# Performance work log

Hardware: AMD Instinct MI355X
Metric: run time of the kernel (lower is better)

Reference implementation:

```python
import jax, jax.numpy as jnp
import numpy as np

B, L, D, H = 4, 1024, 1024, 16
DH = D // H  # 64
TOPK = 32


def setup_inputs() -> dict:
    key = jax.random.key(0)
    ks = jax.random.split(key, 9)
    s = 1.0 / np.sqrt(D)
    return {
        "x": jax.random.normal(ks[0], (B, L, D), jnp.float32),
        "Wq": jax.random.normal(ks[1], (D, D), jnp.float32) * s,
        "bq": jax.random.normal(ks[2], (D,), jnp.float32) * 0.01,
        "Wk": jax.random.normal(ks[3], (D, D), jnp.float32) * s,
        "bk": jax.random.normal(ks[4], (D,), jnp.float32) * 0.01,
        "Wv": jax.random.normal(ks[5], (D, D), jnp.float32) * s,
        "bv": jax.random.normal(ks[6], (D,), jnp.float32) * 0.01,
        "Wo": jax.random.normal(ks[7], (D, D), jnp.float32) * s,
        "bo": jax.random.normal(ks[8], (D,), jnp.float32) * 0.01,
        "top_k": TOPK,
    }


def reference(x, Wq, bq, Wk, bk, Wv, bv, Wo, bo, top_k):
    b, l, _ = x.shape
    q = (x @ Wq + bq).reshape(b, l, H, DH)
    k = (x @ Wk + bk).reshape(b, l, H, DH)
    v = (x @ Wv + bv).reshape(b, l, H, DH)
    # scores: [B, i, j, h]
    scores = jnp.einsum('bihd,bjhd->bijh', q, k) / np.sqrt(DH).astype(np.float32)
    # softmax over axis 2 (j), as in the original (dim=2 of bijh)
    weights = jax.nn.softmax(scores, axis=2)
    if top_k is not None:
        # top-k along j: move j to last axis -> [B, i, h, j]
        w_t = jnp.swapaxes(weights, 2, 3)
        _, idx = jax.lax.top_k(w_t, top_k)
        mask = jnp.put_along_axis(jnp.zeros_like(w_t), idx, 1.0, axis=-1, inplace=False)
        w_t = w_t * mask
        w_t = w_t / (jnp.sum(w_t, axis=-1, keepdims=True) + 1e-8)
        weights = jnp.swapaxes(w_t, 2, 3)
    attn = jnp.einsum('bijh,bjhd->bihd', weights, v).reshape(b, l, D)
    return attn @ Wo + bo
```

## Files before the change

### kernel.cpp

```cpp
#include <hip/hip_runtime.h>
#include <math.h>

#define B_ 4
#define L_ 1024
#define D_ 1024
#define H_ 16
#define DH_ 64
#define M_ (B_*L_)

typedef _Float16 half8 __attribute__((ext_vector_type(8)));
typedef _Float16 half4 __attribute__((ext_vector_type(4)));
typedef float f32x4 __attribute__((ext_vector_type(4)));

#define MFMA16(a,b,c) __builtin_amdgcn_mfma_f32_16x16x32_f16(a, b, c, 0, 0, 0)

__global__ __launch_bounds__(256) void split_x(const float* __restrict__ x,
                                               _Float16* __restrict__ xh,
                                               _Float16* __restrict__ xl) {
  const int i = blockIdx.x * 256 + threadIdx.x;
  float4 v = ((const float4*)x)[i];
  const float a0 = v.x * 16.f, a1 = v.y * 16.f, a2 = v.z * 16.f, a3 = v.w * 16.f;
  const _Float16 h0 = (_Float16)a0, h1 = (_Float16)a1, h2 = (_Float16)a2, h3 = (_Float16)a3;
  half4 hv, lv;
  hv[0] = h0; hv[1] = h1; hv[2] = h2; hv[3] = h3;
  lv[0] = (_Float16)(a0 - (float)h0);
  lv[1] = (_Float16)(a1 - (float)h1);
  lv[2] = (_Float16)(a2 - (float)h2);
  lv[3] = (_Float16)(a3 - (float)h3);
  ((half4*)xh)[i] = hv;
  ((half4*)xl)[i] = lv;
}

__global__ __launch_bounds__(256) void split_wt(const float* __restrict__ W,
                                                _Float16* __restrict__ Wh,
                                                _Float16* __restrict__ Wl) {
  __shared__ float tile[64][65];
  const int t = threadIdx.x;
  const int tk = blockIdx.x & 15;
  const int tn = blockIdx.x >> 4;
  const int kr = t >> 2, ns = (t & 3) * 16;
  const float* src = W + (size_t)(tk * 64 + kr) * D_ + tn * 64 + ns;
  float4 v0 = ((const float4*)src)[0];
  float4 v1 = ((const float4*)src)[1];
  float4 v2 = ((const float4*)src)[2];
  float4 v3 = ((const float4*)src)[3];
  tile[ns + 0][kr] = v0.x;  tile[ns + 1][kr] = v0.y;  tile[ns + 2][kr] = v0.z;  tile[ns + 3][kr] = v0.w;
  tile[ns + 4][kr] = v1.x;  tile[ns + 5][kr] = v1.y;  tile[ns + 6][kr] = v1.z;  tile[ns + 7][kr] = v1.w;
  tile[ns + 8][kr] = v2.x;  tile[ns + 9][kr] = v2.y;  tile[ns + 10][kr] = v2.z; tile[ns + 11][kr] = v2.w;
  tile[ns + 12][kr] = v3.x; tile[ns + 13][kr] = v3.y; tile[ns + 14][kr] = v3.z; tile[ns + 15][kr] = v3.w;
  __syncthreads();
  const int nr = t >> 2, ks = (t & 3) * 16;
  const float* tr = &tile[nr][ks];
  half8 hv0, hv1, lv0, lv1;
#pragma unroll
  for (int i = 0; i < 8; i++) {
    const float s0 = tr[i] * 512.f;
    const float s1 = tr[i + 8] * 512.f;
    const _Float16 h0 = (_Float16)s0, h1 = (_Float16)s1;
    hv0[i] = h0; hv1[i] = h1;
    lv0[i] = (_Float16)(s0 - (float)h0);
    lv1[i] = (_Float16)(s1 - (float)h1);
  }
  _Float16* dh = Wh + (size_t)(tn * 64 + nr) * D_ + tk * 64 + ks;
  _Float16* dl = Wl + (size_t)(tn * 64 + nr) * D_ + tk * 64 + ks;
  *(half8*)dh = hv0; *(half8*)(dh + 8) = hv1;
  *(half8*)dl = lv0; *(half8*)(dl + 8) = lv1;
}

__device__ __forceinline__ void gemm_f16x3_body(
    const _Float16* __restrict__ Ah, const _Float16* __restrict__ Al,
    const _Float16* __restrict__ Bh, const _Float16* __restrict__ Bl,
    const float* __restrict__ bias, float* __restrict__ C) {
  __shared__ __align__(16) _Float16 sA[2][2][128][32];
  __shared__ __align__(16) _Float16 sB[2][2][128][32];
  const int t = threadIdx.x;
  const int lane = t & 63;
  const int wid = t >> 6;
  const int bm = blockIdx.y * 128;
  const int bn = blockIdx.x * 128;

  const int m0 = t >> 2, sp0 = t & 3;
  const int sl0 = sp0 ^ ((m0 >> 1) & 3);
  const int m1 = m0 + 64;
  const _Float16* gA0h = Ah + (size_t)(bm + m0) * D_ + sl0 * 8;
  const _Float16* gA1h = Ah + (size_t)(bm + m1) * D_ + sl0 * 8;
  const _Float16* gA0l = Al + (size_t)(bm + m0) * D_ + sl0 * 8;
  const _Float16* gA1l = Al + (size_t)(bm + m1) * D_ + sl0 * 8;
  const _Float16* gB0h = Bh + (size_t)(bn + m0) * D_ + sl0 * 8;
  const _Float16* gB1h = Bh + (size_t)(bn + m1) * D_ + sl0 * 8;
  const _Float16* gB0l = Bl + (size_t)(bn + m0) * D_ + sl0 * 8;
  const _Float16* gB1l = Bl + (size_t)(bn + m1) * D_ + sl0 * 8;

  half8 rA0h = *(const half8*)(gA0h);
  half8 rA1h = *(const half8*)(gA1h);
  half8 rA0l = *(const half8*)(gA0l);
  half8 rA1l = *(const half8*)(gA1l);
  half8 rB0h = *(const half8*)(gB0h);
  half8 rB1h = *(const half8*)(gB1h);
  half8 rB0l = *(const half8*)(gB0l);
  half8 rB1l = *(const half8*)(gB1l);
  *(half8*)&sA[0][0][m0][sp0 * 8] = rA0h;
  *(half8*)&sA[0][0][m1][sp0 * 8] = rA1h;
  *(half8*)&sA[0][1][m0][sp0 * 8] = rA0l;
  *(half8*)&sA[0][1][m1][sp0 * 8] = rA1l;
  *(half8*)&sB[0][0][m0][sp0 * 8] = rB0h;
  *(half8*)&sB[0][0][m1][sp0 * 8] = rB1h;
  *(half8*)&sB[0][1][m0][sp0 * 8] = rB0l;
  *(half8*)&sB[0][1][m1][sp0 * 8] = rB1l;
  __syncthreads();

  f32x4 acc[4][4];
#pragma unroll
  for (int i = 0; i < 4; i++)
#pragma unroll
    for (int j = 0; j < 4; j++) acc[i][j] = {0.f, 0.f, 0.f, 0.f};

  const int wr = wid >> 1, wc = wid & 1;
  const int l15 = lane & 15;
  const int soff = ((lane >> 4) ^ ((l15 >> 1) & 3)) * 8;

  int p = 0;
  for (int k0 = 0; k0 < 1024; k0 += 32) {
    const bool more = (k0 + 32) < 1024;
    if (more) {
      const int kk = k0 + 32;
      rA0h = *(const half8*)(gA0h + kk);
      rA1h = *(const half8*)(gA1h + kk);
      rA0l = *(const half8*)(gA0l + kk);
      rA1l = *(const half8*)(gA1l + kk);
      rB0h = *(const half8*)(gB0h + kk);
      rB1h = *(const half8*)(gB1h + kk);
      rB0l = *(const half8*)(gB0l + kk);
      rB1l = *(const half8*)(gB1l + kk);
    }
    half8 bh[4], bl[4];
#pragma unroll
    for (int ni = 0; ni < 4; ni++) {
      const int rb = wc * 64 + ni * 16 + l15;
      bh[ni] = *(const half8*)&sB[p][0][rb][soff];
      bl[ni] = *(const half8*)&sB[p][1][rb][soff];
    }
#pragma unroll
    for (int mi = 0; mi < 4; mi++) {
      const int ra = wr * 64 + mi * 16 + l15;
      const half8 ah = *(const half8*)&sA[p][0][ra][soff];
      const half8 al = *(const half8*)&sA[p][1][ra][soff];
#pragma unroll
      for (int ni = 0; ni < 4; ni++) {
        acc[mi][ni] = MFMA16(ah, bh[ni], acc[mi][ni]);
        acc[mi][ni] = MFMA16(ah, bl[ni], acc[mi][ni]);
        acc[mi][ni] = MFMA16(al, bh[ni], acc[mi][ni]);
      }
    }
    if (more) {
      const int q = p ^ 1;
      *(half8*)&sA[q][0][m0][sp0 * 8] = rA0h;
      *(half8*)&sA[q][0][m1][sp0 * 8] = rA1h;
      *(half8*)&sA[q][1][m0][sp0 * 8] = rA0l;
      *(half8*)&sA[q][1][m1][sp0 * 8] = rA1l;
      *(half8*)&sB[q][0][m0][sp0 * 8] = rB0h;
      *(half8*)&sB[q][0][m1][sp0 * 8] = rB1h;
      *(half8*)&sB[q][1][m0][sp0 * 8] = rB0l;
      *(half8*)&sB[q][1][m1][sp0 * 8] = rB1l;
      __syncthreads();
      p = q;
    }
  }

  const float inv = 1.0f / 8192.0f;
  const int orow = bm + wr * 64 + (lane >> 4) * 4;
  const int ocol = bn + wc * 64 + l15;
#pragma unroll
  for (int ni = 0; ni < 4; ni++) {
    const int col = ocol + ni * 16;
    const float bv = bias[col];
#pragma unroll
    for (int mi = 0; mi < 4; mi++) {
      const f32x4 a = acc[mi][ni];
#pragma unroll
      for (int r = 0; r < 4; r++)
        C[(size_t)(orow + mi * 16 + r) * D_ + col] = a[r] * inv + bv;
    }
  }
}

__global__ __launch_bounds__(256, 2) void gemm_qkv_f16(
    const _Float16* __restrict__ xh, const _Float16* __restrict__ xl,
    const _Float16* __restrict__ Whq, const _Float16* __restrict__ Wlq,
    const _Float16* __restrict__ Whk, const _Float16* __restrict__ Wlk,
    const _Float16* __restrict__ Whv, const _Float16* __restrict__ Wlv,
    const float* __restrict__ bq, const float* __restrict__ bk, const float* __restrict__ bv,
    float* __restrict__ qf, float* __restrict__ kf, float* __restrict__ vf) {
  const int z = blockIdx.z;
  const _Float16* Bh = (z == 0) ? Whq : (z == 1) ? Whk : Whv;
  const _Float16* Bl = (z == 0) ? Wlq : (z == 1) ? Wlk : Wlv;
  const float* bias = (z == 0) ? bq : (z == 1) ? bk : bv;
  float* C = (z == 0) ? qf : (z == 1) ? kf : vf;
  gemm_f16x3_body(xh, xl, Bh, Bl, bias, C);
}

__global__ __launch_bounds__(256, 2) void gemm_out_f16(
    const _Float16* __restrict__ ah, const _Float16* __restrict__ al,
    const _Float16* __restrict__ bh, const _Float16* __restrict__ bl,
    const float* __restrict__ bias, float* __restrict__ C) {
  gemm_f16x3_body(ah, al, bh, bl, bias, C);
}

__global__ __launch_bounds__(256) void transpose_k(const float* __restrict__ kf,
                                                   float* __restrict__ kT) {
  __shared__ float tile[64][65];
  const int t = threadIdx.x;
  const int c = blockIdx.x & 15;
  const int h = (blockIdx.x >> 4) & 15;
  const int b = blockIdx.x >> 8;
  const int j0 = c * 64;
  const int jr = t >> 2, ds = (t & 3) * 16;
  const float* src = kf + (size_t)(b * L_ + j0 + jr) * D_ + h * DH_ + ds;
  float4 v0 = ((const float4*)src)[0];
  float4 v1 = ((const float4*)src)[1];
  float4 v2 = ((const float4*)src)[2];
  float4 v3 = ((const float4*)src)[3];
  tile[ds + 0][jr] = v0.x;  tile[ds + 1][jr] = v0.y;  tile[ds + 2][jr] = v0.z;  tile[ds + 3][jr] = v0.w;
  tile[ds + 4][jr] = v1.x;  tile[ds + 5][jr] = v1.y;  tile[ds + 6][jr] = v1.z;  tile[ds + 7][jr] = v1.w;
  tile[ds + 8][jr] = v2.x;  tile[ds + 9][jr] = v2.y;  tile[ds + 10][jr] = v2.z; tile[ds + 11][jr] = v2.w;
  tile[ds + 12][jr] = v3.x; tile[ds + 13][jr] = v3.y; tile[ds + 14][jr] = v3.z; tile[ds + 15][jr] = v3.w;
  __syncthreads();
  const int dr = t >> 2, js = (t & 3) * 16;
  float* dst = kT + ((size_t)((b * 16 + h) * 16 + c)) * 4096 + dr * 64 + js;
  ((float4*)dst)[0] = *(const float4*)&tile[dr][js];
  ((float4*)dst)[1] = *(const float4*)&tile[dr][js + 4];
  ((float4*)dst)[2] = *(const float4*)&tile[dr][js + 8];
  ((float4*)dst)[3] = *(const float4*)&tile[dr][js + 12];
}

#define RFL(x) __int_as_float(__builtin_amdgcn_readfirstlane(__float_as_int(x)))
#define LQROW(r) \
  const float q##r##_0  = RFL(qsh[r][qo +  0]), q##r##_1  = RFL(qsh[r][qo +  1]), \
              q##r##_2  = RFL(qsh[r][qo +  2]), q##r##_3  = RFL(qsh[r][qo +  3]), \
              q##r##_4  = RFL(qsh[r][qo +  4]), q##r##_5  = RFL(qsh[r][qo +  5]), \
              q##r##_6  = RFL(qsh[r][qo +  6]), q##r##_7  = RFL(qsh[r][qo +  7]), \
              q##r##_8  = RFL(qsh[r][qo +  8]), q##r##_9  = RFL(qsh[r][qo +  9]), \
              q##r##_10 = RFL(qsh[r][qo + 10]), q##r##_11 = RFL(qsh[r][qo + 11]), \
              q##r##_12 = RFL(qsh[r][qo + 12]), q##r##_13 = RFL(qsh[r][qo + 13]), \
              q##r##_14 = RFL(qsh[r][qo + 14]), q##r##_15 = RFL(qsh[r][qo + 15]);
#define DOT16(r, sacc) \
  sacc = fmaf(kv0,  q##r##_0,  sacc); sacc = fmaf(kv1,  q##r##_1,  sacc); \
  sacc = fmaf(kv2,  q##r##_2,  sacc); sacc = fmaf(kv3,  q##r##_3,  sacc); \
  sacc = fmaf(kv4,  q##r##_4,  sacc); sacc = fmaf(kv5,  q##r##_5,  sacc); \
  sacc = fmaf(kv6,  q##r##_6,  sacc); sacc = fmaf(kv7,  q##r##_7,  sacc); \
  sacc = fmaf(kv8,  q##r##_8,  sacc); sacc = fmaf(kv9,  q##r##_9,  sacc); \
  sacc = fmaf(kv10, q##r##_10, sacc); sacc = fmaf(kv11, q##r##_11, sacc); \
  sacc = fmaf(kv12, q##r##_12, sacc); sacc = fmaf(kv13, q##r##_13, sacc); \
  sacc = fmaf(kv14, q##r##_14, sacc); sacc = fmaf(kv15, q##r##_15, sacc);

__global__ __launch_bounds__(256, 4) void attn_topk_f32(const float* __restrict__ qf,
                                                        const float* __restrict__ kT,
                                                        const float* __restrict__ vf,
                                                        _Float16* __restrict__ awh,
                                                        _Float16* __restrict__ awl) {
  __shared__ float part2[4][4][64][4];
  __shared__ float qsh[4][64];
  const int t = threadIdx.x;
  const int lane = t & 63;
  const int w = t >> 6;
  const int blk = blockIdx.x;
  const int ib = (blk & 255) * 4;
  const int h = (blk >> 8) & 15;
  const int b = blk >> 12;
  const size_t rowbase = (size_t)b * L_;

  { int r = t >> 6, d = t & 63; qsh[r][d] = qf[(rowbase + ib + r) * D_ + h * DH_ + d]; }
  __syncthreads();

  const int qo = 16 * w;
  LQROW(0) LQROW(1) LQROW(2) LQROW(3)

  const float* ktb = kT + ((size_t)(b * 16 + h) * 16) * 4096 + qo * 64;

  float sc[16];
#pragma unroll
  for (int s = 0; s < 4; ++s) {
#pragma unroll
    for (int c4 = 0; c4 < 4; ++c4) {
      const int c = s * 4 + c4;
      const float* kp = ktb + (size_t)c * 4096 + lane;
      const float kv0 = kp[0 * 64],  kv1 = kp[1 * 64],  kv2 = kp[2 * 64],  kv3 = kp[3 * 64],
                  kv4 = kp[4 * 64],  kv5 = kp[5 * 64],  kv6 = kp[6 * 64],  kv7 = kp[7 * 64],
                  kv8 = kp[8 * 64],  kv9 = kp[9 * 64],  kv10 = kp[10 * 64], kv11 = kp[11 * 64],
                  kv12 = kp[12 * 64], kv13 = kp[13 * 64], kv14 = kp[14 * 64], kv15 = kp[15 * 64];
      float p0 = 0.f, p1 = 0.f, p2 = 0.f, p3 = 0.f;
      DOT16(0, p0) DOT16(1, p1) DOT16(2, p2) DOT16(3, p3)
      part2[c4][0][lane][w] = p0;
      part2[c4][1][lane][w] = p1;
      part2[c4][2][lane][w] = p2;
      part2[c4][3][lane][w] = p3;
    }
    __syncthreads();
#pragma unroll
    for (int c4 = 0; c4 < 4; ++c4) {
      float4 p = *(const float4*)&part2[c4][w][lane][0];
      sc[s * 4 + c4] = ((p.x + p.y) + (p.z + p.w)) * 0.125f;
    }
    __syncthreads();
  }

  float mx = sc[0];
#pragma unroll
  for (int u = 1; u < 16; u++) mx = fmaxf(mx, sc[u]);
#pragma unroll
  for (int off = 32; off >= 1; off >>= 1) mx = fmaxf(mx, __shfl_xor(mx, off, 64));

  float lo = mx - 16.f, hi = mx;
  for (int it = 0; it < 14; ++it) {
    float mid = 0.5f * (lo + hi);
    int cnt = 0;
#pragma unroll
    for (int u = 0; u < 16; u++) cnt += __popcll(__ballot(sc[u] >= mid));
    if (cnt >= 32) lo = mid; else hi = mid;
  }
  int cabove = 0;
#pragma unroll
  for (int u = 0; u < 16; u++) cabove += __popcll(__ballot(sc[u] >= hi));
  float v31 = hi;
  while (cabove < 32) {
    float nx = -INFINITY;
#pragma unroll
    for (int u = 0; u < 16; u++) nx = fmaxf(nx, (sc[u] < v31) ? sc[u] : -INFINITY);
#pragma unroll
    for (int off = 32; off >= 1; off >>= 1) nx = fmaxf(nx, __shfl_xor(nx, off, 64));
    int ceq = 0;
#pragma unroll
    for (int u = 0; u < 16; u++) ceq += __popcll(__ballot(sc[u] == nx));
    cabove += ceq;
    v31 = nx;
  }
  int c_eq = 0;
#pragma unroll
  for (int u = 0; u < 16; u++) c_eq += __popcll(__ballot(sc[u] == v31));
  const int c_gt = cabove - c_eq;
  const bool span = (cabove > 32);
  const int keep_eq = 32 - c_gt;
  float v32;
  if (span) {
    v32 = v31;
  } else {
    float nx = -INFINITY;
#pragma unroll
    for (int u = 0; u < 16; u++) nx = fmaxf(nx, (sc[u] < v31) ? sc[u] : -INFINITY);
#pragma unroll
    for (int off = 32; off >= 1; off >>= 1) nx = fmaxf(nx, __shfl_xor(nx, off, 64));
    v32 = nx;
  }
  const float tau = 0.5f * (v31 + v32);
  const float invbeta = 166666.67f;

  float e[16];
#pragma unroll
  for (int u = 0; u < 16; u++) e[u] = __expf(sc[u] - mx);
  float z = 0.f;
#pragma unroll
  for (int u = 0; u < 16; u++) z += e[u];
#pragma unroll
  for (int off = 32; off >= 1; off >>= 1) z += __shfl_xor(z, off, 64);

  float fw[16];
  if (!span) {
#pragma unroll
    for (int u = 0; u < 16; u++) {
      float arg = (sc[u] - tau) * invbeta;
      fw[u] = (arg > 30.f) ? 1.f : ((arg < -30.f) ? 0.f : 1.f / (1.f + __expf(-arg)));
    }
  }

  const float cutoff = fminf(tau - 1.8e-4f, v31);
  const float* vcol = vf + rowbase * D_ + h * DH_ + lane;
  float S = 0.f, acc = 0.f;
  int eq_seen = 0;
  for (int u = 0; u < 16; ++u) {
    unsigned long long mask = __ballot(sc[u] >= cutoff);
    while (mask) {
      int l2 = (int)__builtin_ctzll(mask);
      mask &= mask - 1;
      float e_ = __shfl(e[u], l2, 64);
      float f_;
      if (span) {
        float s_ = __shfl(sc[u], l2, 64);
        if (s_ > v31) f_ = 1.f;
        else if (s_ == v31) { f_ = (eq_seen < keep_eq) ? 1.f : 0.f; ++eq_seen; }
        else f_ = 0.f;
      } else {
        f_ = __shfl(fw[u], l2, 64);
      }
      float fe = f_ * e_;
      S += fe;
      acc = fmaf(fe, vcol[(size_t)(u * 64 + l2) * D_], acc);
    }
  }
  const float o = acc / (S + 1e-8f * z);
  const float os = o * 16.0f;
  const _Float16 oh = (_Float16)os;
  const size_t oidx = (rowbase + ib + w) * D_ + h * DH_ + lane;
  awh[oidx] = oh;
  awl[oidx] = (_Float16)(os - (float)oh);
}

extern "C" void kernel_launch(void* const* d_in, const int* in_sizes, int n_in,
                              void* d_out, int out_size, void* d_ws, size_t ws_size,
                              hipStream_t stream) {
  const float* x  = (const float*)d_in[0];
  const float* Wq = (const float*)d_in[1];
  const float* bq = (const float*)d_in[2];
  const float* Wk = (const float*)d_in[3];
  const float* bk = (const float*)d_in[4];
  const float* Wv = (const float*)d_in[5];
  const float* bv = (const float*)d_in[6];
  const float* Wo = (const float*)d_in[7];
  const float* bo = (const float*)d_in[8];
  float* out = (float*)d_out;

  const size_t MD = (size_t)M_ * D_;
  const size_t WD = (size_t)D_ * D_;
  float* qf = (float*)d_ws;
  float* kf = qf + MD;
  float* vf = kf + MD;
  float* slotA = vf + MD;
  float* kT = slotA + MD;

  _Float16* xh = (_Float16*)slotA;
  _Float16* xl = xh + MD;
  _Float16* awh = xh;
  _Float16* awl = xl;
  _Float16* Whq = (_Float16*)kT;
  _Float16* Wlq = Whq + WD;
  _Float16* Whk = Wlq + WD;
  _Float16* Wlk = Whk + WD;
  _Float16* Whv = Wlk + WD;
  _Float16* Wlv = Whv + WD;
  _Float16* Who = (_Float16*)kf;
  _Float16* Wlo = Who + WD;

  dim3 b256(256);
  hipLaunchKernelGGL(split_x, dim3(4096), b256, 0, stream, x, xh, xl);
  hipLaunchKernelGGL(split_wt, dim3(256), b256, 0, stream, Wq, Whq, Wlq);
  hipLaunchKernelGGL(split_wt, dim3(256), b256, 0, stream, Wk, Whk, Wlk);
  hipLaunchKernelGGL(split_wt, dim3(256), b256, 0, stream, Wv, Whv, Wlv);
  hipLaunchKernelGGL(gemm_qkv_f16, dim3(8, 32, 3), b256, 0, stream,
                     xh, xl, Whq, Wlq, Whk, Wlk, Whv, Wlv, bq, bk, bv, qf, kf, vf);
  hipLaunchKernelGGL(transpose_k, dim3(1024), b256, 0, stream, kf, kT);
  hipLaunchKernelGGL(split_wt, dim3(256), b256, 0, stream, Wo, Who, Wlo);
  hipLaunchKernelGGL(attn_topk_f32, dim3(16384), b256, 0, stream, qf, kT, vf, awh, awl);
  hipLaunchKernelGGL(gemm_out_f16, dim3(8, 32), b256, 0, stream, awh, awl, Who, Wlo, bo, out);
}
```

Measured before the change: 538.2 us.

## Compute attention scores with split-f16 MFMA and drop the K transpose

The QKV GEMM now writes Q and K directly as scaled hi/lo f16 pairs. A new attention kernel computes the QK^T scores for a 32-row tile with three-term f16 MFMA into a swizzled 128KB LDS score buffer, then runs the same top-k selection and sparse V gather per row. The separate K transpose kernel and the fp32 FMA score loop are removed, and the workspace layout is reorganised. In exchange, the 128KB of LDS per block allows only one 512-thread block per CU, and the split-f16 products may differ slightly from fp32, which could change which 32 keys are selected.

Measured after the change: 732.6 us. +36.1%, slower.

```diff
diff --git a/kernel.cpp b/kernel.cpp
--- a/kernel.cpp
+++ b/kernel.cpp
@@ -70,7 +70,8 @@
 __device__ __forceinline__ void gemm_f16x3_body(
     const _Float16* __restrict__ Ah, const _Float16* __restrict__ Al,
     const _Float16* __restrict__ Bh, const _Float16* __restrict__ Bl,
-    const float* __restrict__ bias, float* __restrict__ C) {
+    const float* __restrict__ bias, float* __restrict__ Cf,
+    _Float16* __restrict__ Ch, _Float16* __restrict__ Cl, const bool f16out) {
   __shared__ __align__(16) _Float16 sA[2][2][128][32];
   __shared__ __align__(16) _Float16 sB[2][2][128][32];
   const int t = threadIdx.x;
@@ -178,8 +179,18 @@
     for (int mi = 0; mi < 4; mi++) {
       const f32x4 a = acc[mi][ni];
 #pragma unroll
-      for (int r = 0; r < 4; r++)
-        C[(size_t)(orow + mi * 16 + r) * D_ + col] = a[r] * inv + bv;
+      for (int r = 0; r < 4; r++) {
+        const size_t idx = (size_t)(orow + mi * 16 + r) * D_ + col;
+        const float val = a[r] * inv + bv;
+        if (f16out) {
+          const float vs = val * 16.0f;
+          const _Float16 hh = (_Float16)vs;
+          Ch[idx] = hh;
+          Cl[idx] = (_Float16)(vs - (float)hh);
+        } else {
+          Cf[idx] = val;
+        }
+      }
     }
   }
 }
@@ -190,218 +201,188 @@
     const _Float16* __restrict__ Whk, const _Float16* __restrict__ Wlk,
     const _Float16* __restrict__ Whv, const _Float16* __restrict__ Wlv,
     const float* __restrict__ bq, const float* __restrict__ bk, const float* __restrict__ bv,
-    float* __restrict__ qf, float* __restrict__ kf, float* __restrict__ vf) {
+    _Float16* __restrict__ qh, _Float16* __restrict__ ql,
+    _Float16* __restrict__ kh, _Float16* __restrict__ kl,
+    float* __restrict__ vf) {
   const int z = blockIdx.z;
   const _Float16* Bh = (z == 0) ? Whq : (z == 1) ? Whk : Whv;
   const _Float16* Bl = (z == 0) ? Wlq : (z == 1) ? Wlk : Wlv;
   const float* bias = (z == 0) ? bq : (z == 1) ? bk : bv;
-  float* C = (z == 0) ? qf : (z == 1) ? kf : vf;
-  gemm_f16x3_body(xh, xl, Bh, Bl, bias, C);
+  if (z == 2) {
+    gemm_f16x3_body(xh, xl, Bh, Bl, bias, vf, nullptr, nullptr, false);
+  } else {
+    _Float16* Ch = (z == 0) ? qh : kh;
+    _Float16* Cl = (z == 0) ? ql : kl;
+    gemm_f16x3_body(xh, xl, Bh, Bl, bias, nullptr, Ch, Cl, true);
+  }
 }
 
 __global__ __launch_bounds__(256, 2) void gemm_out_f16(
     const _Float16* __restrict__ ah, const _Float16* __restrict__ al,
     const _Float16* __restrict__ bh, const _Float16* __restrict__ bl,
     const float* __restrict__ bias, float* __restrict__ C) {
-  gemm_f16x3_body(ah, al, bh, bl, bias, C);
-}
-
-__global__ __launch_bounds__(256) void transpose_k(const float* __restrict__ kf,
-                                                   float* __restrict__ kT) {
-  __shared__ float tile[64][65];
-  const int t = threadIdx.x;
-  const int c = blockIdx.x & 15;
-  const int h = (blockIdx.x >> 4) & 15;
-  const int b = blockIdx.x >> 8;
-  const int j0 = c * 64;
-  const int jr = t >> 2, ds = (t & 3) * 16;
-  const float* src = kf + (size_t)(b * L_ + j0 + jr) * D_ + h * DH_ + ds;
-  float4 v0 = ((const float4*)src)[0];
-  float4 v1 = ((const float4*)src)[1];
-  float4 v2 = ((const float4*)src)[2];
-  float4 v3 = ((const float4*)src)[3];
-  tile[ds + 0][jr] = v0.x;  tile[ds + 1][jr] = v0.y;  tile[ds + 2][jr] = v0.z;  tile[ds + 3][jr] = v0.w;
-  tile[ds + 4][jr] = v1.x;  tile[ds + 5][jr] = v1.y;  tile[ds + 6][jr] = v1.z;  tile[ds + 7][jr] = v1.w;
-  tile[ds + 8][jr] = v2.x;  tile[ds + 9][jr] = v2.y;  tile[ds + 10][jr] = v2.z; tile[ds + 11][jr] = v2.w;
-  tile[ds + 12][jr] = v3.x; tile[ds + 13][jr] = v3.y; tile[ds + 14][jr] = v3.z; tile[ds + 15][jr] = v3.w;
-  __syncthreads();
-  const int dr = t >> 2, js = (t & 3) * 16;
-  float* dst = kT + ((size_t)((b * 16 + h) * 16 + c)) * 4096 + dr * 64 + js;
-  ((float4*)dst)[0] = *(const float4*)&tile[dr][js];
-  ((float4*)dst)[1] = *(const float4*)&tile[dr][js + 4];
-  ((float4*)dst)[2] = *(const float4*)&tile[dr][js + 8];
-  ((float4*)dst)[3] = *(const float4*)&tile[dr][js + 12];
-}
-
-#define RFL(x) __int_as_float(__builtin_amdgcn_readfirstlane(__float_as_int(x)))
-#define LQROW(r) \
-  const float q##r##_0  = RFL(qsh[r][qo +  0]), q##r##_1  = RFL(qsh[r][qo +  1]), \
-              q##r##_2  = RFL(qsh[r][qo +  2]), q##r##_3  = RFL(qsh[r][qo +  3]), \
-              q##r##_4  = RFL(qsh[r][qo +  4]), q##r##_5  = RFL(qsh[r][qo +  5]), \
-              q##r##_6  = RFL(qsh[r][qo +  6]), q##r##_7  = RFL(qsh[r][qo +  7]), \
-              q##r##_8  = RFL(qsh[r][qo +  8]), q##r##_9  = RFL(qsh[r][qo +  9]), \
-              q##r##_10 = RFL(qsh[r][qo + 10]), q##r##_11 = RFL(qsh[r][qo + 11]), \
-              q##r##_12 = RFL(qsh[r][qo + 12]), q##r##_13 = RFL(qsh[r][qo + 13]), \
-              q##r##_14 = RFL(qsh[r][qo + 14]), q##r##_15 = RFL(qsh[r][qo + 15]);
-#define DOT16(r, sacc) \
-  sacc = fmaf(kv0,  q##r##_0,  sacc); sacc = fmaf(kv1,  q##r##_1,  sacc); \
-  sacc = fmaf(kv2,  q##r##_2,  sacc); sacc = fmaf(kv3,  q##r##_3,  sacc); \
-  sacc = fmaf(kv4,  q##r##_4,  sacc); sacc = fmaf(kv5,  q##r##_5,  sacc); \
-  sacc = fmaf(kv6,  q##r##_6,  sacc); sacc = fmaf(kv7,  q##r##_7,  sacc); \
-  sacc = fmaf(kv8,  q##r##_8,  sacc); sacc = fmaf(kv9,  q##r##_9,  sacc); \
-  sacc = fmaf(kv10, q##r##_10, sacc); sacc = fmaf(kv11, q##r##_11, sacc); \
-  sacc = fmaf(kv12, q##r##_12, sacc); sacc = fmaf(kv13, q##r##_13, sacc); \
-  sacc = fmaf(kv14, q##r##_14, sacc); sacc = fmaf(kv15, q##r##_15, sacc);
-
-__global__ __launch_bounds__(256, 4) void attn_topk_f32(const float* __restrict__ qf,
-                                                        const float* __restrict__ kT,
-                                                        const float* __restrict__ vf,
-                                                        _Float16* __restrict__ awh,
-                                                        _Float16* __restrict__ awl) {
-  __shared__ float part2[4][4][64][4];
-  __shared__ float qsh[4][64];
+  gemm_f16x3_body(ah, al, bh, bl, bias, C, nullptr, nullptr, false);
+}
+
+#define SSWZ(row) (((row) & 7) << 2)
+
+__global__ __launch_bounds__(512, 1) void attn_topk_mfma(
+    const _Float16* __restrict__ qh, const _Float16* __restrict__ ql,
+    const _Float16* __restrict__ kh, const _Float16* __restrict__ kl,
+    const float* __restrict__ vf,
+    _Float16* __restrict__ awh, _Float16* __restrict__ awl) {
+  __shared__ float S[32][1024];
   const int t = threadIdx.x;
   const int lane = t & 63;
   const int w = t >> 6;
-  const int blk = blockIdx.x;
-  const int ib = (blk & 255) * 4;
-  const int h = (blk >> 8) & 15;
-  const int b = blk >> 12;
+  const int i0 = blockIdx.x * 32;
+  const int h = blockIdx.y;
+  const int b = blockIdx.z;
   const size_t rowbase = (size_t)b * L_;
-
-  { int r = t >> 6, d = t & 63; qsh[r][d] = qf[(rowbase + ib + r) * D_ + h * DH_ + d]; }
+  const int l15 = lane & 15;
+  const int kgrp = lane >> 4;
+
+  half8 Ahf[2][2], Alf[2][2];
+#pragma unroll
+  for (int rt = 0; rt < 2; rt++)
+#pragma unroll
+    for (int ks = 0; ks < 2; ks++) {
+      const size_t off = (rowbase + i0 + rt * 16 + l15) * D_ + h * DH_ + ks * 32 + kgrp * 8;
+      Ahf[rt][ks] = *(const half8*)(qh + off);
+      Alf[rt][ks] = *(const half8*)(ql + off);
+    }
+
+  const float sscale = 1.0f / 2048.0f;
+  for (int jt = 0; jt < 8; jt++) {
+    const int j0 = w * 128 + jt * 16;
+    const size_t koff = (rowbase + j0 + l15) * D_ + h * DH_ + kgrp * 8;
+    const half8 Bh0 = *(const half8*)(kh + koff);
+    const half8 Bh1 = *(const half8*)(kh + koff + 32);
+    const half8 Bl0 = *(const half8*)(kl + koff);
+    const half8 Bl1 = *(const half8*)(kl + koff + 32);
+#pragma unroll
+    for (int rt = 0; rt < 2; rt++) {
+      f32x4 acc = {0.f, 0.f, 0.f, 0.f};
+      acc = MFMA16(Ahf[rt][0], Bh0, acc);
+      acc = MFMA16(Ahf[rt][1], Bh1, acc);
+      acc = MFMA16(Ahf[rt][0], Bl0, acc);
+      acc = MFMA16(Ahf[rt][1], Bl1, acc);
+      acc = MFMA16(Alf[rt][0], Bh0, acc);
+      acc = MFMA16(Alf[rt][1], Bh1, acc);
+      const int srow = rt * 16 + kgrp * 4;
+#pragma unroll
+      for (int r = 0; r < 4; r++)
+        S[srow + r][(j0 + l15) ^ SSWZ(srow + r)] = acc[r] * sscale;
+    }
+  }
   __syncthreads();
 
-  const int qo = 16 * w;
-  LQROW(0) LQROW(1) LQROW(2) LQROW(3)
-
-  const float* ktb = kT + ((size_t)(b * 16 + h) * 16) * 4096 + qo * 64;
-
-  float sc[16];
-#pragma unroll
-  for (int s = 0; s < 4; ++s) {
-#pragma unroll
-    for (int c4 = 0; c4 < 4; ++c4) {
-      const int c = s * 4 + c4;
-      const float* kp = ktb + (size_t)c * 4096 + lane;
-      const float kv0 = kp[0 * 64],  kv1 = kp[1 * 64],  kv2 = kp[2 * 64],  kv3 = kp[3 * 64],
-                  kv4 = kp[4 * 64],  kv5 = kp[5 * 64],  kv6 = kp[6 * 64],  kv7 = kp[7 * 64],
-                  kv8 = kp[8 * 64],  kv9 = kp[9 * 64],  kv10 = kp[10 * 64], kv11 = kp[11 * 64],
-                  kv12 = kp[12 * 64], kv13 = kp[13 * 64], kv14 = kp[14 * 64], kv15 = kp[15 * 64];
-      float p0 = 0.f, p1 = 0.f, p2 = 0.f, p3 = 0.f;
-      DOT16(0, p0) DOT16(1, p1) DOT16(2, p2) DOT16(3, p3)
-      part2[c4][0][lane][w] = p0;
-      part2[c4][1][lane][w] = p1;
-      part2[c4][2][lane][w] = p2;
-      part2[c4][3][lane][w] = p3;
-    }
-    __syncthreads();
-#pragma unroll
-    for (int c4 = 0; c4 < 4; ++c4) {
-      float4 p = *(const float4*)&part2[c4][w][lane][0];
-      sc[s * 4 + c4] = ((p.x + p.y) + (p.z + p.w)) * 0.125f;
-    }
-    __syncthreads();
-  }
-
-  float mx = sc[0];
-#pragma unroll
-  for (int u = 1; u < 16; u++) mx = fmaxf(mx, sc[u]);
-#pragma unroll
-  for (int off = 32; off >= 1; off >>= 1) mx = fmaxf(mx, __shfl_xor(mx, off, 64));
-
-  float lo = mx - 16.f, hi = mx;
-  for (int it = 0; it < 14; ++it) {
-    float mid = 0.5f * (lo + hi);
-    int cnt = 0;
-#pragma unroll
-    for (int u = 0; u < 16; u++) cnt += __popcll(__ballot(sc[u] >= mid));
-    if (cnt >= 32) lo = mid; else hi = mid;
-  }
-  int cabove = 0;
-#pragma unroll
-  for (int u = 0; u < 16; u++) cabove += __popcll(__ballot(sc[u] >= hi));
-  float v31 = hi;
-  while (cabove < 32) {
-    float nx = -INFINITY;
-#pragma unroll
-    for (int u = 0; u < 16; u++) nx = fmaxf(nx, (sc[u] < v31) ? sc[u] : -INFINITY);
-#pragma unroll
-    for (int off = 32; off >= 1; off >>= 1) nx = fmaxf(nx, __shfl_xor(nx, off, 64));
-    int ceq = 0;
-#pragma unroll
-    for (int u = 0; u < 16; u++) ceq += __popcll(__ballot(sc[u] == nx));
-    cabove += ceq;
-    v31 = nx;
-  }
-  int c_eq = 0;
-#pragma unroll
-  for (int u = 0; u < 16; u++) c_eq += __popcll(__ballot(sc[u] == v31));
-  const int c_gt = cabove - c_eq;
-  const bool span = (cabove > 32);
-  const int keep_eq = 32 - c_gt;
-  float v32;
-  if (span) {
-    v32 = v31;
-  } else {
-    float nx = -INFINITY;
-#pragma unroll
-    for (int u = 0; u < 16; u++) nx = fmaxf(nx, (sc[u] < v31) ? sc[u] : -INFINITY);
-#pragma unroll
-    for (int off = 32; off >= 1; off >>= 1) nx = fmaxf(nx, __shfl_xor(nx, off, 64));
-    v32 = nx;
-  }
-  const float tau = 0.5f * (v31 + v32);
-  const float invbeta = 166666.67f;
-
-  float e[16];
-#pragma unroll
-  for (int u = 0; u < 16; u++) e[u] = __expf(sc[u] - mx);
-  float z = 0.f;
-#pragma unroll
-  for (int u = 0; u < 16; u++) z += e[u];
-#pragma unroll
-  for (int off = 32; off >= 1; off >>= 1) z += __shfl_xor(z, off, 64);
-
-  float fw[16];
-  if (!span) {
-#pragma unroll
-    for (int u = 0; u < 16; u++) {
-      float arg = (sc[u] - tau) * invbeta;
-      fw[u] = (arg > 30.f) ? 1.f : ((arg < -30.f) ? 0.f : 1.f / (1.f + __expf(-arg)));
-    }
-  }
-
-  const float cutoff = fminf(tau - 1.8e-4f, v31);
-  const float* vcol = vf + rowbase * D_ + h * DH_ + lane;
-  float S = 0.f, acc = 0.f;
-  int eq_seen = 0;
-  for (int u = 0; u < 16; ++u) {
-    unsigned long long mask = __ballot(sc[u] >= cutoff);
-    while (mask) {
-      int l2 = (int)__builtin_ctzll(mask);
-      mask &= mask - 1;
-      float e_ = __shfl(e[u], l2, 64);
-      float f_;
-      if (span) {
-        float s_ = __shfl(sc[u], l2, 64);
-        if (s_ > v31) f_ = 1.f;
-        else if (s_ == v31) { f_ = (eq_seen < keep_eq) ? 1.f : 0.f; ++eq_seen; }
-        else f_ = 0.f;
-      } else {
-        f_ = __shfl(fw[u], l2, 64);
+  for (int rr = 0; rr < 4; rr++) {
+    const int row = w * 4 + rr;
+    const int swz = SSWZ(row);
+    float sc[16];
+#pragma unroll
+    for (int u = 0; u < 16; u++) sc[u] = S[row][(u * 64 + lane) ^ swz];
+
+    float mx = sc[0];
+#pragma unroll
+    for (int u = 1; u < 16; u++) mx = fmaxf(mx, sc[u]);
+#pragma unroll
+    for (int off = 32; off >= 1; off >>= 1) mx = fmaxf(mx, __shfl_xor(mx, off, 64));
+
+    float lo = mx - 16.f, hi = mx;
+    for (int it = 0; it < 14; ++it) {
+      float mid = 0.5f * (lo + hi);
+      int cnt = 0;
+#pragma unroll
+      for (int u = 0; u < 16; u++) cnt += __popcll(__ballot(sc[u] >= mid));
+      if (cnt >= 32) lo = mid; else hi = mid;
+    }
+    int cabove = 0;
+#pragma unroll
+    for (int u = 0; u < 16; u++) cabove += __popcll(__ballot(sc[u] >= hi));
+    float v31 = hi;
+    while (cabove < 32) {
+      float nx = -INFINITY;
+#pragma unroll
+      for (int u = 0; u < 16; u++) nx = fmaxf(nx, (sc[u] < v31) ? sc[u] : -INFINITY);
+#pragma unroll
+      for (int off = 32; off >= 1; off >>= 1) nx = fmaxf(nx, __shfl_xor(nx, off, 64));
+      int ceq = 0;
+#pragma unroll
+      for (int u = 0; u < 16; u++) ceq += __popcll(__ballot(sc[u] == nx));
+      cabove += ceq;
+      v31 = nx;
+    }
+    int c_eq = 0;
+#pragma unroll
+    for (int u = 0; u < 16; u++) c_eq += __popcll(__ballot(sc[u] == v31));
+    const int c_gt = cabove - c_eq;
+    const bool span = (cabove > 32);
+    const int keep_eq = 32 - c_gt;
+    float v32;
+    if (span) {
+      v32 = v31;
+    } else {
+      float nx = -INFINITY;
+#pragma unroll
+      for (int u = 0; u < 16; u++) nx = fmaxf(nx, (sc[u] < v31) ? sc[u] : -INFINITY);
+#pragma unroll
+      for (int off = 32; off >= 1; off >>= 1) nx = fmaxf(nx, __shfl_xor(nx, off, 64));
+      v32 = nx;
+    }
+    const float tau = 0.5f * (v31 + v32);
+    const float invbeta = 166666.67f;
+
+    float e[16];
+#pragma unroll
+    for (int u = 0; u < 16; u++) e[u] = __expf(sc[u] - mx);
+    float z = 0.f;
+#pragma unroll
+    for (int u = 0; u < 16; u++) z += e[u];
+#pragma unroll
+    for (int off = 32; off >= 1; off >>= 1) z += __shfl_xor(z, off, 64);
+
+    float fw[16];
+    if (!span) {
+#pragma unroll
+      for (int u = 0; u < 16; u++) {
+        float arg = (sc[u] - tau) * invbeta;
+        fw[u] = (arg > 30.f) ? 1.f : ((arg < -30.f) ? 0.f : 1.f / (1.f + __expf(-arg)));
       }
-      float fe = f_ * e_;
-      S += fe;
-      acc = fmaf(fe, vcol[(size_t)(u * 64 + l2) * D_], acc);
-    }
-  }
-  const float o = acc / (S + 1e-8f * z);
-  const float os = o * 16.0f;
-  const _Float16 oh = (_Float16)os;
-  const size_t oidx = (rowbase + ib + w) * D_ + h * DH_ + lane;
-  awh[oidx] = oh;
-  awl[oidx] = (_Float16)(os - (float)oh);
+    }
+
+    const float cutoff = fminf(tau - 1.8e-4f, v31);
+    const float* vcol = vf + rowbase * D_ + h * DH_ + lane;
+    float Ssum = 0.f, acc = 0.f;
+    int eq_seen = 0;
+    for (int u = 0; u < 16; ++u) {
+      unsigned long long mask = __ballot(sc[u] >= cutoff);
+      while (mask) {
+        int l2 = (int)__builtin_ctzll(mask);
+        mask &= mask - 1;
+        float e_ = __shfl(e[u], l2, 64);
+        float f_;
+        if (span) {
+          float s_ = __shfl(sc[u], l2, 64);
+          if (s_ > v31) f_ = 1.f;
+          else if (s_ == v31) { f_ = (eq_seen < keep_eq) ? 1.f : 0.f; ++eq_seen; }
+          else f_ = 0.f;
+        } else {
+          f_ = __shfl(fw[u], l2, 64);
+        }
+        float fe = f_ * e_;
+        Ssum += fe;
+        acc = fmaf(fe, vcol[(size_t)(u * 64 + l2) * D_], acc);
+      }
+    }
+    const float o = acc / (Ssum + 1e-8f * z);
+    const float os = o * 16.0f;
+    const _Float16 oh = (_Float16)os;
+    const size_t oidx = (rowbase + i0 + row) * D_ + h * DH_ + lane;
+    awh[oidx] = oh;
+    awl[oidx] = (_Float16)(os - (float)oh);
+  }
 }
 
 extern "C" void kernel_launch(void* const* d_in, const int* in_sizes, int n_in,
@@ -420,23 +401,24 @@
 
   const size_t MD = (size_t)M_ * D_;
   const size_t WD = (size_t)D_ * D_;
-  float* qf = (float*)d_ws;
-  float* kf = qf + MD;
-  float* vf = kf + MD;
-  float* slotA = vf + MD;
-  float* kT = slotA + MD;
-
-  _Float16* xh = (_Float16*)slotA;
-  _Float16* xl = xh + MD;
+  float* slot0 = (float*)d_ws;
+  float* slot1 = slot0 + MD;
+  float* vf    = slot1 + MD;
+  float* slot3 = vf + MD;
+  float* slot4 = slot3 + MD;
+
+  _Float16* qh = (_Float16*)slot0;  _Float16* ql = qh + MD;
+  _Float16* kh = (_Float16*)slot1;  _Float16* kl = kh + MD;
+  _Float16* xh = (_Float16*)slot3;  _Float16* xl = xh + MD;
   _Float16* awh = xh;
   _Float16* awl = xl;
-  _Float16* Whq = (_Float16*)kT;
+  _Float16* Whq = (_Float16*)slot4;
   _Float16* Wlq = Whq + WD;
   _Float16* Whk = Wlq + WD;
   _Float16* Wlk = Whk + WD;
   _Float16* Whv = Wlk + WD;
   _Float16* Wlv = Whv + WD;
-  _Float16* Who = (_Float16*)kf;
+  _Float16* Who = Wlv + WD;
   _Float16* Wlo = Who + WD;
 
   dim3 b256(256);
@@ -444,10 +426,12 @@
   hipLaunchKernelGGL(split_wt, dim3(256), b256, 0, stream, Wq, Whq, Wlq);
   hipLaunchKernelGGL(split_wt, dim3(256), b256, 0, stream, Wk, Whk, Wlk);
   hipLaunchKernelGGL(split_wt, dim3(256), b256, 0, stream, Wv, Whv, Wlv);
+  hipLaunchKernelGGL(split_wt, dim3(256), b256, 0, stream, Wo, Who, Wlo);
   hipLaunchKernelGGL(gemm_qkv_f16, dim3(8, 32, 3), b256, 0, stream,
-                     xh, xl, Whq, Wlq, Whk, Wlk, Whv, Wlv, bq, bk, bv, qf, kf, vf);
-  hipLaunchKernelGGL(transpose_k, dim3(1024), b256, 0, stream, kf, kT);
-  hipLaunchKernelGGL(split_wt, dim3(256), b256, 0, stream, Wo, Who, Wlo);
-  hipLaunchKernelGGL(attn_topk_f32, dim3(16384), b256, 0, stream, qf, kT, vf, awh, awl);
-  hipLaunchKernelGGL(gemm_out_f16, dim3(8, 32), b256, 0, stream, awh, awl, Who, Wlo, bo, out);
-}
+                     xh, xl, Whq, Wlq, Whk, Wlk, Whv, Wlv, bq, bk, bv,
+                     qh, ql, kh, kl, vf);
+  hipLaunchKernelGGL(attn_topk_mfma, dim3(32, 16, 4), dim3(512), 0, stream,
+                     qh, ql, kh, kl, vf, awh, awl);
+  hipLaunchKernelGGL(gemm_out_f16, dim3(8, 32), b256, 0, stream,
+                     awh, awl, Who, Wlo, bo, out);
+}
```
